# Kernel tuning notes

Measured on AMD Instinct MI355X. Metric: run time of the kernel, lower is better.

## Reference

```python
import jax, jax.numpy as jnp
import numpy as np

EMBED_DIM = 128
NUM_SYMBOLS = 200000
PAD = NUM_SYMBOLS
B = 1024          # query batch
FEW = 5           # support set size
NB = 200          # neighbors per entity (fixed by module docstring)
D_MODEL = 2 * EMBED_DIM       # 256
D_INNER = 2 * D_MODEL         # 512
HID = 2 * D_MODEL             # LSTMCell hidden = 2*input_dim = 512
STEPS = 4                     # process_steps
LN_EPS = 1e-5


def setup_inputs() -> dict:
    key = jax.random.key(0)
    ks = jax.random.split(key, 16)

    def conn(k, n):
        c = jax.random.randint(k, (n, NB, 2), 0, NUM_SYMBOLS, dtype=jnp.int64)
        # pad last 50 neighbor slots so the masked max-pool path is exercised
        return c.at[:, 150:, :].set(PAD)

    inp = {
        "query_left_connections": conn(ks[0], B),
        "query_right_connections": conn(ks[1], B),
        "support_left_connections": conn(ks[2], FEW),
        "support_right_connections": conn(ks[3], FEW),
        "query_left_degrees": jax.random.randint(ks[4], (B,), 1, NB, dtype=jnp.int32),
        "query_right_degrees": jax.random.randint(ks[5], (B,), 1, NB, dtype=jnp.int32),
        "support_left_degrees": jax.random.randint(ks[6], (FEW,), 1, NB, dtype=jnp.int32),
        "support_right_degrees": jax.random.randint(ks[7], (FEW,), 1, NB, dtype=jnp.int32),
    }

    # parameters (eval mode: dropout disabled)
    emb = jax.random.normal(ks[8], (NUM_SYMBOLS + 1, EMBED_DIM), jnp.float32) * 0.02
    inp["emb"] = emb.at[PAD].set(0.0)              # padding_idx row is zero
    inp["gcn_W"] = jax.random.normal(ks[9], (EMBED_DIM, 2 * EMBED_DIM), jnp.float32) * 0.05
    inp["gcn_wb"] = jnp.zeros((EMBED_DIM,), jnp.float32)   # gcn_w linear bias
    inp["gcn_b"] = jnp.zeros((EMBED_DIM,), jnp.float32)    # extra gcn_b param (init constant 0)
    inp["proj1_W"] = jax.random.normal(ks[10], (D_INNER, D_MODEL), jnp.float32) * 0.05
    inp["proj1_b"] = jnp.zeros((D_INNER,), jnp.float32)
    inp["proj2_W"] = jax.random.normal(ks[11], (D_MODEL, D_INNER), jnp.float32) * 0.05
    inp["proj2_b"] = jnp.zeros((D_MODEL,), jnp.float32)
    inp["ln_g"] = jnp.ones((D_MODEL,), jnp.float32)
    inp["ln_b"] = jnp.zeros((D_MODEL,), jnp.float32)
    inp["W_ih"] = jax.random.normal(ks[12], (4 * HID, D_MODEL), jnp.float32) * 0.04
    inp["W_hh"] = jax.random.normal(ks[13], (4 * HID, HID), jnp.float32) * 0.04
    inp["b_ih"] = jnp.zeros((4 * HID,), jnp.float32)
    inp["b_hh"] = jnp.zeros((4 * HID,), jnp.float32)
    return inp


def _neighbor_encoder(conn, emb, gcn_W, gcn_wb, gcn_b):
    # conn: (n, NB, 2) ints; gather embed + concat + linear + leaky_relu + masked max + tanh
    rel, ent = conn[:, :, 0], conn[:, :, 1]
    pad_mask = (rel == PAD) | (ent == PAD)                      # (n, NB)
    x = jnp.concatenate([emb[rel], emb[ent]], axis=-1)          # (n, NB, 2E)
    p = jnp.einsum('nke,de->nkd', x, gcn_W) + gcn_wb + gcn_b    # (n, NB, E)
    p = jax.nn.leaky_relu(p, negative_slope=0.1)
    p = jnp.where(pad_mask[:, :, None], -jnp.inf, p)
    return jnp.tanh(jnp.max(p, axis=1))                         # (n, E)


def _support_encoder(x, p1W, p1b, p2W, p2b, g, b):
    # FFN with residual + LayerNorm (GMatching SupportEncoder), dropout off in eval
    h = jax.nn.relu(x @ p1W.T + p1b)
    o = h @ p2W.T + p2b + x
    mu = jnp.mean(o, axis=-1, keepdims=True)
    var = jnp.var(o, axis=-1, keepdims=True)
    return (o - mu) / jnp.sqrt(var + LN_EPS) * g + b


def _query_encoder(support, query, W_ih, W_hh, b_ih, b_hh):
    # GMatching QueryEncoder: LSTMCell attention, `process_steps` iterations
    # support: (1, D_MODEL), query: (bq, D_MODEL)
    bq = query.shape[0]
    h_r = jnp.zeros((bq, HID), query.dtype)
    c = jnp.zeros((bq, HID), query.dtype)
    h = query
    for _ in range(STEPS):
        gates = query @ W_ih.T + b_ih + h_r @ W_hh.T + b_hh     # (bq, 4*HID)
        i, f, g, o = jnp.split(gates, 4, axis=-1)
        c = jax.nn.sigmoid(f) * c + jax.nn.sigmoid(i) * jnp.tanh(g)
        h_new = jax.nn.sigmoid(o) * jnp.tanh(c)                 # (bq, HID)
        h = query + h_new[:, :D_MODEL]
        attn = jax.nn.softmax(h @ support.T, axis=1)            # (bq, 1)
        r = attn @ support                                      # (bq, D_MODEL)
        h_r = jnp.concatenate([h, r], axis=1)
    return h


def reference(query_left_connections, query_right_connections,
              support_left_connections, support_right_connections,
              query_left_degrees, query_right_degrees,
              support_left_degrees, support_right_degrees,
              emb, gcn_W, gcn_wb, gcn_b,
              proj1_W, proj1_b, proj2_W, proj2_b, ln_g, ln_b,
              W_ih, W_hh, b_ih, b_hh):
    ql = _neighbor_encoder(query_left_connections, emb, gcn_W, gcn_wb, gcn_b)
    qr = _neighbor_encoder(query_right_connections, emb, gcn_W, gcn_wb, gcn_b)
    sl = _neighbor_encoder(support_left_connections, emb, gcn_W, gcn_wb, gcn_b)
    sr = _neighbor_encoder(support_right_connections, emb, gcn_W, gcn_wb, gcn_b)
    query_neighbor = jnp.concatenate([ql, qr], axis=-1)      # (B, D_MODEL)
    support_neighbor = jnp.concatenate([sl, sr], axis=-1)    # (FEW, D_MODEL)

    support_g = _support_encoder(support_neighbor[None], proj1_W, proj1_b, proj2_W, proj2_b, ln_g, ln_b)
    support_g = jnp.mean(support_g, axis=1)                  # (1, D_MODEL)
    query_g = _support_encoder(query_neighbor[:, None, :], proj1_W, proj1_b, proj2_W, proj2_b, ln_g, ln_b)
    query_g = query_g[:, 0, :]                               # (B, D_MODEL)

    query_f = _query_encoder(support_g, query_g, W_ih, W_hh, b_ih, b_hh)  # (B, D_MODEL)
    return (query_f @ support_g.T)[:, 0]                     # (B,)
```

## Files before the change

kernel.cpp:

```cpp
#include <hip/hip_runtime.h>
#include <math.h>

#define EMBED   128
#define DMODEL  256
#define DINNER  512
#define HIDN    512
#define NBK     200
#define BQ      1024
#define FEW     5
#define PAD_IDX 200000
#define LN_EPS  1e-5f
#define NTILES  7

typedef short          s16x4  __attribute__((ext_vector_type(4)));
typedef short          s16x8  __attribute__((ext_vector_type(8)));
typedef float          f32x4  __attribute__((ext_vector_type(4)));
typedef float          f32x16 __attribute__((ext_vector_type(16)));
typedef unsigned int   u32;
typedef unsigned short u16;

__device__ __forceinline__ float sigmoidf_(float x) { return 1.0f / (1.0f + expf(-x)); }

__device__ __forceinline__ u32 f2bf(float f) {
    u32 u = __builtin_bit_cast(u32, f);
    u += 0x7fffu + ((u >> 16) & 1u);
    return u >> 16;
}
__device__ __forceinline__ s16x8 pack8(float4 a, float4 b) {
    typedef u32 u32x4_ __attribute__((ext_vector_type(4)));
    u32x4_ q;
    q.x = f2bf(a.x) | (f2bf(a.y) << 16);
    q.y = f2bf(a.z) | (f2bf(a.w) << 16);
    q.z = f2bf(b.x) | (f2bf(b.y) << 16);
    q.w = f2bf(b.z) | (f2bf(b.w) << 16);
    return __builtin_bit_cast(s16x8, q);
}

__global__ __launch_bounds__(256) void convert_weights_kernel(
    const float* __restrict__ W_ih, const float* __restrict__ W_hh,
    const float* __restrict__ p1W,  const float* __restrict__ p2W,
    u16* __restrict__ wih_bf, u16* __restrict__ whh_bf,
    u16* __restrict__ p1_bf,  u16* __restrict__ p2_bf)
{
    int gid = blockIdx.x * 256 + threadIdx.x;
    const float* src; u16* dst; int local, stride, KS, liveRemap;
    if (gid < 32768)      { local = gid;          src = W_ih; dst = wih_bf; stride = 256; KS = 8;  liveRemap = 1; }
    else if (gid < 65536) { local = gid - 32768;  src = W_hh; dst = whh_bf; stride = 512; KS = 8;  liveRemap = 1; }
    else if (gid < 81920) { local = gid - 65536;  src = p1W;  dst = p1_bf;  stride = 256; KS = 8;  liveRemap = 0; }
    else                  { local = gid - 81920;  src = p2W;  dst = p2_bf;  stride = 512; KS = 16; liveRemap = 0; }
    int lane = local & 63;
    int ts   = local >> 6;
    int ks   = ts & (KS - 1);
    int tile = ts / KS;
    int n  = tile * 16 + (lane & 15);
    int kb = ks * 32 + (lane >> 4) * 8;
    int row = liveRemap ? ((n >> 8) * 512 + (n & 255)) : n;
    const float* sp = src + (size_t)row * stride + kb;
    float4 x0 = *(const float4*)sp;
    float4 x1 = *(const float4*)(sp + 4);
    *(s16x8*)(dst + (size_t)local * 8) = pack8(x0, x1);
}

__global__ __launch_bounds__(256) void neighbor_kernel(
    const int* __restrict__ qlc, const int* __restrict__ qrc,
    const int* __restrict__ slc, const int* __restrict__ src_,
    const float* __restrict__ emb, const float* __restrict__ W,
    const float* __restrict__ wb,  const float* __restrict__ bb,
    float* __restrict__ qn, float* __restrict__ sn)
{
    int b = blockIdx.x;
    const int* conn; float* out; int n; int side;
    if (b < BQ)                { conn = qlc;  n = b;            side = 0; out = qn; }
    else if (b < 2*BQ)         { conn = qrc;  n = b - BQ;       side = 1; out = qn; }
    else if (b < 2*BQ + FEW)   { conn = slc;  n = b - 2*BQ;     side = 0; out = sn; }
    else                       { conn = src_; n = b - 2*BQ-FEW; side = 1; out = sn; }

    int t = threadIdx.x;
    int w = t >> 6, l = t & 63;
    int d0 = w * 32;
    int m31 = l & 31, half = l >> 5;

    __shared__ __align__(16) u32 bs[64 * 66];

    s16x8 afrag[16];
    const float* wrow = W + (d0 + m31) * DMODEL + half * 8;
    #pragma unroll
    for (int ks = 0; ks < 16; ++ks) {
        float4 x0 = *(const float4*)(wrow + ks * 16);
        float4 x1 = *(const float4*)(wrow + ks * 16 + 4);
        afrag[ks] = pack8(x0, x1);
    }

    const int* crow = conn + n * NBK * 2;
    u32 vmask = 0;
    #pragma unroll
    for (int nt = 0; nt < NTILES; ++nt) {
        int krow = nt * 32 + m31;
        if (krow < NBK) {
            int rel = crow[2 * krow], ent = crow[2 * krow + 1];
            if (rel != PAD_IDX && ent != PAD_IDX) vmask |= (1u << nt);
        }
    }

    int gr = t >> 2;
    int gq = t & 3;
    int g_is_ent = (gr >= 32);
    int g_m = gr & 31;

    int srcrow[NTILES];
    #pragma unroll
    for (int nt = 0; nt < NTILES; ++nt) {
        int krow = nt * 32 + g_m;
        int rel = PAD_IDX, ent = PAD_IDX;
        if (krow < NBK) { rel = crow[2 * krow]; ent = crow[2 * krow + 1]; }
        int gvalid = (rel != PAD_IDX) && (ent != PAD_IDX);
        srcrow[nt] = gvalid ? (g_is_ent ? ent : rel) : PAD_IDX;
    }

    int tl[NTILES]; int ntl = 0;
    #pragma unroll
    for (int nt = 0; nt < NTILES; ++nt)
        if (__any((int)((vmask >> nt) & 1u))) tl[ntl++] = nt;

    float vm[16];
    #pragma unroll
    for (int r = 0; r < 16; ++r) vm[r] = -INFINITY;

    u32* dst = bs + gr * 66 + gq * 16;
    const u32* rrel = bs + m31 * 66 + half * 4;
    const u32* rent = bs + (32 + m31) * 66 + half * 4;

    float4 f[8];
    if (ntl > 0) {
        const float4* gp = (const float4*)(emb + (size_t)srcrow[tl[0]] * EMBED + gq * 32);
        #pragma unroll
        for (int i = 0; i < 8; ++i) f[i] = gp[i];
    }

    for (int i = 0; i < ntl; ++i) {
        int nt = tl[i];
        __syncthreads();
        #pragma unroll
        for (int j = 0; j < 8; ++j) {
            dst[2 * j]     = f2bf(f[j].x) | (f2bf(f[j].y) << 16);
            dst[2 * j + 1] = f2bf(f[j].z) | (f2bf(f[j].w) << 16);
        }
        __syncthreads();

        float4 f2[8];
        if (i + 1 < ntl) {
            const float4* gp = (const float4*)(emb + (size_t)srcrow[tl[i + 1]] * EMBED + gq * 32);
            #pragma unroll
            for (int j = 0; j < 8; ++j) f2[j] = gp[j];
        }

        f32x16 acc0 = {0.f,0.f,0.f,0.f,0.f,0.f,0.f,0.f,0.f,0.f,0.f,0.f,0.f,0.f,0.f,0.f};
        f32x16 acc1 = acc0;
        #pragma unroll
        for (int ks = 0; ks < 8; ++ks) {
            s16x4 lo = *(const s16x4*)(rrel + ks * 8);
            s16x4 hi = *(const s16x4*)(rrel + ks * 8 + 2);
            s16x8 bf = __builtin_shufflevector(lo, hi, 0, 1, 2, 3, 4, 5, 6, 7);
            acc0 = __builtin_amdgcn_mfma_f32_32x32x16_bf16(afrag[ks], bf, acc0, 0, 0, 0);
        }
        #pragma unroll
        for (int ks = 0; ks < 8; ++ks) {
            s16x4 lo = *(const s16x4*)(rent + ks * 8);
            s16x4 hi = *(const s16x4*)(rent + ks * 8 + 2);
            s16x8 bf = __builtin_shufflevector(lo, hi, 0, 1, 2, 3, 4, 5, 6, 7);
            acc1 = __builtin_amdgcn_mfma_f32_32x32x16_bf16(afrag[8 + ks], bf, acc1, 0, 0, 0);
        }
        int cvalid = (vmask >> nt) & 1;
        #pragma unroll
        for (int r = 0; r < 16; ++r) {
            float v = cvalid ? (acc0[r] + acc1[r]) : -INFINITY;
            vm[r] = fmaxf(vm[r], v);
        }
        #pragma unroll
        for (int j = 0; j < 8; ++j) f[j] = f2[j];
    }

    #pragma unroll
    for (int off = 1; off < 32; off <<= 1) {
        #pragma unroll
        for (int r = 0; r < 16; ++r)
            vm[r] = fmaxf(vm[r], __shfl_xor(vm[r], off, 64));
    }

    if (m31 == 0) {
        #pragma unroll
        for (int r = 0; r < 16; ++r) {
            int d = d0 + (r & 3) + 8 * (r >> 2) + 4 * half;
            float p = vm[r] + wb[d] + bb[d];
            p = (p >= 0.f) ? p : 0.1f * p;
            out[n * DMODEL + side * EMBED + d] = tanhf(p);
        }
    }
}

__global__ __launch_bounds__(256) void support_enc_kernel(
    const float* __restrict__ qn, const float* __restrict__ sn,
    const u16* __restrict__ p1_bf, const float* __restrict__ p1b,
    const u16* __restrict__ p2_bf, const float* __restrict__ p2b,
    const float* __restrict__ lng, const float* __restrict__ lnb,
    float* __restrict__ query_g, float* __restrict__ sup_ln)
{
    __shared__ __align__(16) float xs[16][260];
    __shared__ __align__(16) float hsd[16][516];
    __shared__ __align__(16) float os[16][260];
    int t = threadIdx.x;
    int w = t >> 6, l = t & 63;
    int r0 = blockIdx.x * 16;

    for (int r = 0; r < 16; ++r) {
        int row = r0 + r;
        float v = 0.f;
        if (row < BQ + FEW)
            v = (row < BQ) ? qn[row * DMODEL + t] : sn[(row - BQ) * DMODEL + t];
        xs[r][t] = v;
    }
    __syncthreads();

    int am = l & 15, ak = (l >> 4) * 8;

    s16x8 a1[8];
    #pragma unroll
    for (int ks = 0; ks < 8; ++ks) {
        float4 x0 = *(const float4*)&xs[am][ks * 32 + ak];
        float4 x1 = *(const float4*)&xs[am][ks * 32 + ak + 4];
        a1[ks] = pack8(x0, x1);
    }

    #pragma unroll
    for (int j = 0; j < 8; ++j) {
        int nt = w * 8 + j;
        f32x4 acc = {0.f, 0.f, 0.f, 0.f};
        const u16* bp = p1_bf + (size_t)nt * 4096 + l * 8;
        #pragma unroll
        for (int ks = 0; ks < 8; ++ks) {
            s16x8 bf = *(const s16x8*)(bp + ks * 512);
            acc = __builtin_amdgcn_mfma_f32_16x16x32_bf16(a1[ks], bf, acc, 0, 0, 0);
        }
        int nn = nt * 16 + (l & 15);
        float bj = p1b[nn];
        #pragma unroll
        for (int reg = 0; reg < 4; ++reg) {
            int m = (l >> 4) * 4 + reg;
            hsd[m][nn] = fmaxf(acc[reg] + bj, 0.f);
        }
    }
    __syncthreads();

    s16x8 a2[16];
    #pragma unroll
    for (int ks = 0; ks < 16; ++ks) {
        float4 x0 = *(const float4*)&hsd[am][ks * 32 + ak];
        float4 x1 = *(const float4*)&hsd[am][ks * 32 + ak + 4];
        a2[ks] = pack8(x0, x1);
    }

    #pragma unroll
    for (int j = 0; j < 4; ++j) {
        int nt = w * 4 + j;
        f32x4 acc = {0.f, 0.f, 0.f, 0.f};
        const u16* bp = p2_bf + (size_t)nt * 8192 + l * 8;
        #pragma unroll
        for (int ks = 0; ks < 16; ++ks) {
            s16x8 bf = *(const s16x8*)(bp + ks * 512);
            acc = __builtin_amdgcn_mfma_f32_16x16x32_bf16(a2[ks], bf, acc, 0, 0, 0);
        }
        int nn = nt * 16 + (l & 15);
        float bj = p2b[nn];
        #pragma unroll
        for (int reg = 0; reg < 4; ++reg) {
            int m = (l >> 4) * 4 + reg;
            os[m][nn] = acc[reg] + bj + xs[m][nn];
        }
    }
    __syncthreads();

    for (int j = 0; j < 4; ++j) {
        int m = w * 4 + j;
        float sum = 0.f, sq = 0.f;
        #pragma unroll
        for (int i = 0; i < 4; ++i) {
            float v = os[m][l + 64 * i];
            sum += v; sq += v * v;
        }
        for (int off = 32; off; off >>= 1) {
            sum += __shfl_xor(sum, off, 64);
            sq  += __shfl_xor(sq,  off, 64);
        }
        float mu  = sum * (1.f / DMODEL);
        float var = sq * (1.f / DMODEL) - mu * mu;
        float inv = rsqrtf(var + LN_EPS);
        int row = r0 + m;
        if (row < BQ + FEW) {
            float* outp = (row < BQ) ? (query_g + row * DMODEL) : (sup_ln + (row - BQ) * DMODEL);
            #pragma unroll
            for (int i = 0; i < 4; ++i) {
                int dd = l + 64 * i;
                outp[dd] = (os[m][dd] - mu) * inv * lng[dd] + lnb[dd];
            }
        }
    }
}

__global__ __launch_bounds__(256) void sWp_kernel(
    const float* __restrict__ sup_ln, const float* __restrict__ W_hh,
    float* __restrict__ sWp)
{
    int w = threadIdx.x >> 6, l = threadIdx.x & 63;
    int wave_id = blockIdx.x * 4 + w;
    float se[4];
    #pragma unroll
    for (int j = 0; j < 4; ++j) {
        float a = 0.f;
        for (int i = 0; i < FEW; ++i) a += sup_ln[i * DMODEL + l + 64 * j];
        se[j] = a * (1.f / FEW);
    }
    for (int i = 0; i < 4; ++i) {
        int p = wave_id * 4 + i;
        int pp = p >> 8, q = p & 255;
        const float* wr = W_hh + (size_t)(pp * 512 + q) * HIDN + 256;
        float part = 0.f;
        #pragma unroll
        for (int j = 0; j < 4; ++j) part += se[j] * wr[l + 64 * j];
        for (int off = 32; off; off >>= 1) part += __shfl_xor(part, off, 64);
        if (l == 0) sWp[p] = part;
    }
}

__global__ __launch_bounds__(256) void lstm_mfma_kernel(
    const float* __restrict__ query_g, const float* __restrict__ sup_ln,
    const float* __restrict__ sWp, const u16* __restrict__ wih_bf,
    const u16* __restrict__ whh_bf, const float* __restrict__ b_ih,
    const float* __restrict__ b_hh, float* __restrict__ out)
{
    __shared__ __align__(16) float qs[16][260];
    __shared__ __align__(16) float hs[16][260];
    __shared__ float sv[DMODEL];
    int t = threadIdx.x;
    int w = t >> 6, l = t & 63;
    int n0 = blockIdx.x * 16;

    {
        float a = 0.f;
        for (int i = 0; i < FEW; ++i) a += sup_ln[i * DMODEL + t];
        sv[t] = a * (1.f / FEW);
    }
    for (int r = 0; r < 16; ++r) qs[r][t] = query_g[(size_t)(n0 + r) * DMODEL + t];
    __syncthreads();

    int am = l & 15, ak = (l >> 4) * 8;

    s16x8 af[8];
    #pragma unroll
    for (int ks = 0; ks < 8; ++ks) {
        float4 x0 = *(const float4*)&qs[am][ks * 32 + ak];
        float4 x1 = *(const float4*)&qs[am][ks * 32 + ak + 4];
        af[ks] = pack8(x0, x1);
    }

    f32x4 base[4][4];
    #pragma unroll
    for (int pp = 0; pp < 4; ++pp) {
        #pragma unroll
        for (int qt = 0; qt < 4; ++qt) {
            int tp = pp * 16 + w * 4 + qt;
            f32x4 acc = {0.f, 0.f, 0.f, 0.f};
            const u16* bp = wih_bf + (size_t)tp * 4096 + l * 8;
            #pragma unroll
            for (int ks = 0; ks < 8; ++ks) {
                s16x8 bf = *(const s16x8*)(bp + ks * 512);
                acc = __builtin_amdgcn_mfma_f32_16x16x32_bf16(af[ks], bf, acc, 0, 0, 0);
            }
            base[pp][qt] = acc;
        }
    }
    #pragma unroll
    for (int pp = 0; pp < 4; ++pp) {
        #pragma unroll
        for (int qt = 0; qt < 4; ++qt) {
            int q = w * 64 + qt * 16 + (l & 15);
            float bsv = b_ih[pp * 512 + q] + b_hh[pp * 512 + q];
            base[pp][qt].x += bsv; base[pp][qt].y += bsv;
            base[pp][qt].z += bsv; base[pp][qt].w += bsv;
        }
    }

    float c[4][4];
    #pragma unroll
    for (int qt = 0; qt < 4; ++qt) {
        int q = w * 64 + qt * 16 + (l & 15);
        #pragma unroll
        for (int reg = 0; reg < 4; ++reg) {
            int m = (l >> 4) * 4 + reg;
            float gi = base[0][qt][reg];
            float gg = base[2][qt][reg];
            float go = base[3][qt][reg];
            float cc = sigmoidf_(gi) * tanhf(gg);
            c[qt][reg] = cc;
            hs[m][q] = qs[m][q] + sigmoidf_(go) * tanhf(cc);
        }
    }
    #pragma unroll
    for (int pp = 0; pp < 4; ++pp) {
        #pragma unroll
        for (int qt = 0; qt < 4; ++qt) {
            int q = w * 64 + qt * 16 + (l & 15);
            float sw = sWp[pp * 256 + q];
            base[pp][qt].x += sw; base[pp][qt].y += sw;
            base[pp][qt].z += sw; base[pp][qt].w += sw;
        }
    }
    __syncthreads();

    for (int st = 1; st < 4; ++st) {
        #pragma unroll
        for (int ks = 0; ks < 8; ++ks) {
            float4 x0 = *(const float4*)&hs[am][ks * 32 + ak];
            float4 x1 = *(const float4*)&hs[am][ks * 32 + ak + 4];
            af[ks] = pack8(x0, x1);
        }
        __syncthreads();

        f32x4 gacc[4][4];
        #pragma unroll
        for (int pp = 0; pp < 4; ++pp) {
            #pragma unroll
            for (int qt = 0; qt < 4; ++qt) {
                int tp = pp * 16 + w * 4 + qt;
                f32x4 acc = base[pp][qt];
                const u16* bp = whh_bf + (size_t)tp * 4096 + l * 8;
                #pragma unroll
                for (int ks = 0; ks < 8; ++ks) {
                    s16x8 bf = *(const s16x8*)(bp + ks * 512);
                    acc = __builtin_amdgcn_mfma_f32_16x16x32_bf16(af[ks], bf, acc, 0, 0, 0);
                }
                gacc[pp][qt] = acc;
            }
        }
        #pragma unroll
        for (int qt = 0; qt < 4; ++qt) {
            int q = w * 64 + qt * 16 + (l & 15);
            #pragma unroll
            for (int reg = 0; reg < 4; ++reg) {
                int m = (l >> 4) * 4 + reg;
                float gi = gacc[0][qt][reg];
                float gf = gacc[1][qt][reg];
                float gg = gacc[2][qt][reg];
                float go = gacc[3][qt][reg];
                float cc = sigmoidf_(gf) * c[qt][reg] + sigmoidf_(gi) * tanhf(gg);
                c[qt][reg] = cc;
                hs[m][q] = qs[m][q] + sigmoidf_(go) * tanhf(cc);
            }
        }
        __syncthreads();
    }

    for (int j = 0; j < 4; ++j) {
        int m = w * 4 + j;
        float part = 0.f;
        #pragma unroll
        for (int i = 0; i < 4; ++i) {
            int e = l + 64 * i;
            part += hs[m][e] * sv[e];
        }
        for (int off = 32; off; off >>= 1) part += __shfl_xor(part, off, 64);
        if (l == 0) out[n0 + m] = part;
    }
}

extern "C" void kernel_launch(void* const* d_in, const int* in_sizes, int n_in,
                              void* d_out, int out_size, void* d_ws, size_t ws_size,
                              hipStream_t stream)
{
    const int*   qlc  = (const int*)d_in[0];
    const int*   qrc  = (const int*)d_in[1];
    const int*   slc  = (const int*)d_in[2];
    const int*   src_ = (const int*)d_in[3];
    const float* emb   = (const float*)d_in[8];
    const float* gcnW  = (const float*)d_in[9];
    const float* gcnwb = (const float*)d_in[10];
    const float* gcnb  = (const float*)d_in[11];
    const float* p1W   = (const float*)d_in[12];
    const float* p1b   = (const float*)d_in[13];
    const float* p2W   = (const float*)d_in[14];
    const float* p2b   = (const float*)d_in[15];
    const float* lng   = (const float*)d_in[16];
    const float* lnb   = (const float*)d_in[17];
    const float* W_ih  = (const float*)d_in[18];
    const float* W_hh  = (const float*)d_in[19];
    const float* b_ih  = (const float*)d_in[20];
    const float* b_hh  = (const float*)d_in[21];
    float* out = (float*)d_out;

    char* ws = (char*)d_ws;
    float* qn      = (float*)(ws + 0);
    float* sn      = (float*)(ws + 1048576);
    float* query_g = (float*)(ws + 1053696);
    float* sup_ln  = (float*)(ws + 2102272);
    float* sWp     = (float*)(ws + 2107392);
    u16*   wih_bf  = (u16*)(ws + 2111488);
    u16*   whh_bf  = (u16*)(ws + 2635776);
    u16*   p1_bf   = (u16*)(ws + 3160064);
    u16*   p2_bf   = (u16*)(ws + 3422208);
    (void)ws_size; (void)in_sizes; (void)n_in; (void)out_size;

    convert_weights_kernel<<<384, 256, 0, stream>>>(
        W_ih, W_hh, p1W, p2W, wih_bf, whh_bf, p1_bf, p2_bf);
    neighbor_kernel<<<2 * BQ + 2 * FEW, 256, 0, stream>>>(
        qlc, qrc, slc, src_, emb, gcnW, gcnwb, gcnb, qn, sn);
    support_enc_kernel<<<(BQ + FEW + 15) / 16, 256, 0, stream>>>(
        qn, sn, p1_bf, p1b, p2_bf, p2b, lng, lnb, query_g, sup_ln);
    sWp_kernel<<<64, 256, 0, stream>>>(sup_ln, W_hh, sWp);
    lstm_mfma_kernel<<<BQ / 16, 256, 0, stream>>>(
        query_g, sup_ln, sWp, wih_bf, whh_bf, b_ih, b_hh, out);
}
```

Baseline: 410.8 us.

## Gather bf16 embeddings directly into MFMA fragments and widen encoder/LSTM blocks

```diff
diff --git a/kernel.cpp b/kernel.cpp
--- a/kernel.cpp
+++ b/kernel.cpp
@@ -12,7 +12,10 @@
 #define LN_EPS  1e-5f
 #define NTILES  7
 
-typedef short          s16x4  __attribute__((ext_vector_type(4)));
+#define EMB_ELEMS 25600128
+#define EMB_THREADS (EMB_ELEMS / 8)
+#define EMB_BLOCKS ((EMB_THREADS + 255) / 256)
+
 typedef short          s16x8  __attribute__((ext_vector_type(8)));
 typedef float          f32x4  __attribute__((ext_vector_type(4)));
 typedef float          f32x16 __attribute__((ext_vector_type(16)));
@@ -36,13 +39,26 @@
     return __builtin_bit_cast(s16x8, q);
 }
 
-__global__ __launch_bounds__(256) void convert_weights_kernel(
+__global__ __launch_bounds__(256) void convert_all_kernel(
     const float* __restrict__ W_ih, const float* __restrict__ W_hh,
     const float* __restrict__ p1W,  const float* __restrict__ p2W,
+    const float* __restrict__ emb,
     u16* __restrict__ wih_bf, u16* __restrict__ whh_bf,
-    u16* __restrict__ p1_bf,  u16* __restrict__ p2_bf)
+    u16* __restrict__ p1_bf,  u16* __restrict__ p2_bf,
+    u16* __restrict__ emb_bf)
 {
-    int gid = blockIdx.x * 256 + threadIdx.x;
+    int bid = blockIdx.x;
+    if (bid >= 384) {
+        size_t gid = (size_t)(bid - 384) * 256 + threadIdx.x;
+        if (gid < EMB_THREADS) {
+            size_t base = gid * 8;
+            float4 x0 = *(const float4*)(emb + base);
+            float4 x1 = *(const float4*)(emb + base + 4);
+            *(s16x8*)(emb_bf + base) = pack8(x0, x1);
+        }
+        return;
+    }
+    int gid = bid * 256 + threadIdx.x;
     const float* src; u16* dst; int local, stride, KS, liveRemap;
     if (gid < 32768)      { local = gid;          src = W_ih; dst = wih_bf; stride = 256; KS = 8;  liveRemap = 1; }
     else if (gid < 65536) { local = gid - 32768;  src = W_hh; dst = whh_bf; stride = 512; KS = 8;  liveRemap = 1; }
@@ -61,10 +77,12 @@
     *(s16x8*)(dst + (size_t)local * 8) = pack8(x0, x1);
 }
 
+template<bool BF>
 __global__ __launch_bounds__(256) void neighbor_kernel(
     const int* __restrict__ qlc, const int* __restrict__ qrc,
     const int* __restrict__ slc, const int* __restrict__ src_,
-    const float* __restrict__ emb, const float* __restrict__ W,
+    const float* __restrict__ emb, const u16* __restrict__ emb_bf,
+    const float* __restrict__ W,
     const float* __restrict__ wb,  const float* __restrict__ bb,
     float* __restrict__ qn, float* __restrict__ sn)
 {
@@ -80,8 +98,6 @@
     int d0 = w * 32;
     int m31 = l & 31, half = l >> 5;
 
-    __shared__ __align__(16) u32 bs[64 * 66];
-
     s16x8 afrag[16];
     const float* wrow = W + (d0 + m31) * DMODEL + half * 8;
     #pragma unroll
@@ -91,93 +107,57 @@
         afrag[ks] = pack8(x0, x1);
     }
 
-    const int* crow = conn + n * NBK * 2;
+    const int2* crow = (const int2*)(conn + n * NBK * 2);
+    int srel[NTILES], sent[NTILES];
     u32 vmask = 0;
     #pragma unroll
     for (int nt = 0; nt < NTILES; ++nt) {
         int krow = nt * 32 + m31;
-        if (krow < NBK) {
-            int rel = crow[2 * krow], ent = crow[2 * krow + 1];
-            if (rel != PAD_IDX && ent != PAD_IDX) vmask |= (1u << nt);
-        }
-    }
-
-    int gr = t >> 2;
-    int gq = t & 3;
-    int g_is_ent = (gr >= 32);
-    int g_m = gr & 31;
-
-    int srcrow[NTILES];
-    #pragma unroll
+        int rel = PAD_IDX, ent = PAD_IDX;
+        if (krow < NBK) { int2 re = crow[krow]; rel = re.x; ent = re.y; }
+        int v = (rel != PAD_IDX) && (ent != PAD_IDX);
+        if (v) vmask |= (1u << nt);
+        srel[nt] = v ? rel : PAD_IDX;
+        sent[nt] = v ? ent : PAD_IDX;
+    }
+
+    float vm[16];
+    #pragma unroll
+    for (int r = 0; r < 16; ++r) vm[r] = -INFINITY;
+
     for (int nt = 0; nt < NTILES; ++nt) {
-        int krow = nt * 32 + g_m;
-        int rel = PAD_IDX, ent = PAD_IDX;
-        if (krow < NBK) { rel = crow[2 * krow]; ent = crow[2 * krow + 1]; }
-        int gvalid = (rel != PAD_IDX) && (ent != PAD_IDX);
-        srcrow[nt] = gvalid ? (g_is_ent ? ent : rel) : PAD_IDX;
-    }
-
-    int tl[NTILES]; int ntl = 0;
-    #pragma unroll
-    for (int nt = 0; nt < NTILES; ++nt)
-        if (__any((int)((vmask >> nt) & 1u))) tl[ntl++] = nt;
-
-    float vm[16];
-    #pragma unroll
-    for (int r = 0; r < 16; ++r) vm[r] = -INFINITY;
-
-    u32* dst = bs + gr * 66 + gq * 16;
-    const u32* rrel = bs + m31 * 66 + half * 4;
-    const u32* rent = bs + (32 + m31) * 66 + half * 4;
-
-    float4 f[8];
-    if (ntl > 0) {
-        const float4* gp = (const float4*)(emb + (size_t)srcrow[tl[0]] * EMBED + gq * 32);
-        #pragma unroll
-        for (int i = 0; i < 8; ++i) f[i] = gp[i];
-    }
-
-    for (int i = 0; i < ntl; ++i) {
-        int nt = tl[i];
-        __syncthreads();
-        #pragma unroll
-        for (int j = 0; j < 8; ++j) {
-            dst[2 * j]     = f2bf(f[j].x) | (f2bf(f[j].y) << 16);
-            dst[2 * j + 1] = f2bf(f[j].z) | (f2bf(f[j].w) << 16);
-        }
-        __syncthreads();
-
-        float4 f2[8];
-        if (i + 1 < ntl) {
-            const float4* gp = (const float4*)(emb + (size_t)srcrow[tl[i + 1]] * EMBED + gq * 32);
-            #pragma unroll
-            for (int j = 0; j < 8; ++j) f2[j] = gp[j];
-        }
-
-        f32x16 acc0 = {0.f,0.f,0.f,0.f,0.f,0.f,0.f,0.f,0.f,0.f,0.f,0.f,0.f,0.f,0.f,0.f};
-        f32x16 acc1 = acc0;
-        #pragma unroll
-        for (int ks = 0; ks < 8; ++ks) {
-            s16x4 lo = *(const s16x4*)(rrel + ks * 8);
-            s16x4 hi = *(const s16x4*)(rrel + ks * 8 + 2);
-            s16x8 bf = __builtin_shufflevector(lo, hi, 0, 1, 2, 3, 4, 5, 6, 7);
-            acc0 = __builtin_amdgcn_mfma_f32_32x32x16_bf16(afrag[ks], bf, acc0, 0, 0, 0);
-        }
-        #pragma unroll
-        for (int ks = 0; ks < 8; ++ks) {
-            s16x4 lo = *(const s16x4*)(rent + ks * 8);
-            s16x4 hi = *(const s16x4*)(rent + ks * 8 + 2);
-            s16x8 bf = __builtin_shufflevector(lo, hi, 0, 1, 2, 3, 4, 5, 6, 7);
-            acc1 = __builtin_amdgcn_mfma_f32_32x32x16_bf16(afrag[8 + ks], bf, acc1, 0, 0, 0);
-        }
-        int cvalid = (vmask >> nt) & 1;
+        if (!__any((int)((vmask >> nt) & 1u))) continue;
+
+        s16x8 bfr[16];
+        if (BF) {
+            const u16* pr = emb_bf + (size_t)srel[nt] * EMBED + half * 8;
+            const u16* pe = emb_bf + (size_t)sent[nt] * EMBED + half * 8;
+            #pragma unroll
+            for (int ks = 0; ks < 8; ++ks) bfr[ks]     = *(const s16x8*)(pr + ks * 16);
+            #pragma unroll
+            for (int ks = 0; ks < 8; ++ks) bfr[8 + ks] = *(const s16x8*)(pe + ks * 16);
+        } else {
+            const float* pr = emb + (size_t)srel[nt] * EMBED + half * 8;
+            const float* pe = emb + (size_t)sent[nt] * EMBED + half * 8;
+            #pragma unroll
+            for (int ks = 0; ks < 8; ++ks)
+                bfr[ks] = pack8(*(const float4*)(pr + ks * 16), *(const float4*)(pr + ks * 16 + 4));
+            #pragma unroll
+            for (int ks = 0; ks < 8; ++ks)
+                bfr[8 + ks] = pack8(*(const float4*)(pe + ks * 16), *(const float4*)(pe + ks * 16 + 4));
+        }
+
+        f32x16 acc = {0.f,0.f,0.f,0.f,0.f,0.f,0.f,0.f,0.f,0.f,0.f,0.f,0.f,0.f,0.f,0.f};
+        #pragma unroll
+        for (int j = 0; j < 16; ++j)
+            acc = __builtin_amdgcn_mfma_f32_32x32x16_bf16(afrag[j], bfr[j], acc, 0, 0, 0);
+
+        int cv = (vmask >> nt) & 1;
         #pragma unroll
         for (int r = 0; r < 16; ++r) {
-            float v = cvalid ? (acc0[r] + acc1[r]) : -INFINITY;
+            float v = cv ? acc[r] : -INFINITY;
             vm[r] = fmaxf(vm[r], v);
         }
-        #pragma unroll
-        for (int j = 0; j < 8; ++j) f[j] = f2[j];
     }
 
     #pragma unroll
@@ -198,7 +178,7 @@
     }
 }
 
-__global__ __launch_bounds__(256) void support_enc_kernel(
+__global__ __launch_bounds__(512) void support_enc_kernel(
     const float* __restrict__ qn, const float* __restrict__ sn,
     const u16* __restrict__ p1_bf, const float* __restrict__ p1b,
     const u16* __restrict__ p2_bf, const float* __restrict__ p2b,
@@ -212,12 +192,15 @@
     int w = t >> 6, l = t & 63;
     int r0 = blockIdx.x * 16;
 
-    for (int r = 0; r < 16; ++r) {
+    #pragma unroll
+    for (int j = 0; j < 8; ++j) {
+        int idx = j * 512 + t;
+        int r = idx >> 8, cc = idx & 255;
         int row = r0 + r;
         float v = 0.f;
         if (row < BQ + FEW)
-            v = (row < BQ) ? qn[row * DMODEL + t] : sn[(row - BQ) * DMODEL + t];
-        xs[r][t] = v;
+            v = (row < BQ) ? qn[(size_t)row * DMODEL + cc] : sn[(size_t)(row - BQ) * DMODEL + cc];
+        xs[r][cc] = v;
     }
     __syncthreads();
 
@@ -232,8 +215,8 @@
     }
 
     #pragma unroll
-    for (int j = 0; j < 8; ++j) {
-        int nt = w * 8 + j;
+    for (int j = 0; j < 4; ++j) {
+        int nt = w * 4 + j;
         f32x4 acc = {0.f, 0.f, 0.f, 0.f};
         const u16* bp = p1_bf + (size_t)nt * 4096 + l * 8;
         #pragma unroll
@@ -260,8 +243,8 @@
     }
 
     #pragma unroll
-    for (int j = 0; j < 4; ++j) {
-        int nt = w * 4 + j;
+    for (int j = 0; j < 2; ++j) {
+        int nt = w * 2 + j;
         f32x4 acc = {0.f, 0.f, 0.f, 0.f};
         const u16* bp = p2_bf + (size_t)nt * 8192 + l * 8;
         #pragma unroll
@@ -279,8 +262,8 @@
     }
     __syncthreads();
 
-    for (int j = 0; j < 4; ++j) {
-        int m = w * 4 + j;
+    for (int j = 0; j < 2; ++j) {
+        int m = w * 2 + j;
         float sum = 0.f, sq = 0.f;
         #pragma unroll
         for (int i = 0; i < 4; ++i) {
@@ -296,7 +279,7 @@
         float inv = rsqrtf(var + LN_EPS);
         int row = r0 + m;
         if (row < BQ + FEW) {
-            float* outp = (row < BQ) ? (query_g + row * DMODEL) : (sup_ln + (row - BQ) * DMODEL);
+            float* outp = (row < BQ) ? (query_g + (size_t)row * DMODEL) : (sup_ln + (size_t)(row - BQ) * DMODEL);
             #pragma unroll
             for (int i = 0; i < 4; ++i) {
                 int dd = l + 64 * i;
@@ -331,7 +314,7 @@
     }
 }
 
-__global__ __launch_bounds__(256) void lstm_mfma_kernel(
+__global__ __launch_bounds__(512) void lstm_mfma_kernel(
     const float* __restrict__ query_g, const float* __restrict__ sup_ln,
     const float* __restrict__ sWp, const u16* __restrict__ wih_bf,
     const u16* __restrict__ whh_bf, const float* __restrict__ b_ih,
@@ -344,12 +327,17 @@
     int w = t >> 6, l = t & 63;
     int n0 = blockIdx.x * 16;
 
-    {
+    if (t < DMODEL) {
         float a = 0.f;
         for (int i = 0; i < FEW; ++i) a += sup_ln[i * DMODEL + t];
         sv[t] = a * (1.f / FEW);
     }
-    for (int r = 0; r < 16; ++r) qs[r][t] = query_g[(size_t)(n0 + r) * DMODEL + t];
+    #pragma unroll
+    for (int j = 0; j < 8; ++j) {
+        int idx = j * 512 + t;
+        int r = idx >> 8, cc = idx & 255;
+        qs[r][cc] = query_g[(size_t)(n0 + r) * DMODEL + cc];
+    }
     __syncthreads();
 
     int am = l & 15, ak = (l >> 4) * 8;
@@ -362,12 +350,12 @@
         af[ks] = pack8(x0, x1);
     }
 
-    f32x4 base[4][4];
+    f32x4 base[4][2];
     #pragma unroll
     for (int pp = 0; pp < 4; ++pp) {
         #pragma unroll
-        for (int qt = 0; qt < 4; ++qt) {
-            int tp = pp * 16 + w * 4 + qt;
+        for (int qt = 0; qt < 2; ++qt) {
+            int tp = pp * 16 + 2 * w + qt;
             f32x4 acc = {0.f, 0.f, 0.f, 0.f};
             const u16* bp = wih_bf + (size_t)tp * 4096 + l * 8;
             #pragma unroll
@@ -381,18 +369,18 @@
     #pragma unroll
     for (int pp = 0; pp < 4; ++pp) {
         #pragma unroll
-        for (int qt = 0; qt < 4; ++qt) {
-            int q = w * 64 + qt * 16 + (l & 15);
+        for (int qt = 0; qt < 2; ++qt) {
+            int q = w * 32 + qt * 16 + (l & 15);
             float bsv = b_ih[pp * 512 + q] + b_hh[pp * 512 + q];
             base[pp][qt].x += bsv; base[pp][qt].y += bsv;
             base[pp][qt].z += bsv; base[pp][qt].w += bsv;
         }
     }
 
-    float c[4][4];
-    #pragma unroll
-    for (int qt = 0; qt < 4; ++qt) {
-        int q = w * 64 + qt * 16 + (l & 15);
+    float c[2][4];
+    #pragma unroll
+    for (int qt = 0; qt < 2; ++qt) {
+        int q = w * 32 + qt * 16 + (l & 15);
         #pragma unroll
         for (int reg = 0; reg < 4; ++reg) {
             int m = (l >> 4) * 4 + reg;
@@ -407,8 +395,8 @@
     #pragma unroll
     for (int pp = 0; pp < 4; ++pp) {
         #pragma unroll
-        for (int qt = 0; qt < 4; ++qt) {
-            int q = w * 64 + qt * 16 + (l & 15);
+        for (int qt = 0; qt < 2; ++qt) {
+            int q = w * 32 + qt * 16 + (l & 15);
             float sw = sWp[pp * 256 + q];
             base[pp][qt].x += sw; base[pp][qt].y += sw;
             base[pp][qt].z += sw; base[pp][qt].w += sw;
@@ -425,12 +413,12 @@
         }
         __syncthreads();
 
-        f32x4 gacc[4][4];
+        f32x4 gacc[4][2];
         #pragma unroll
         for (int pp = 0; pp < 4; ++pp) {
             #pragma unroll
-            for (int qt = 0; qt < 4; ++qt) {
-                int tp = pp * 16 + w * 4 + qt;
+            for (int qt = 0; qt < 2; ++qt) {
+                int tp = pp * 16 + 2 * w + qt;
                 f32x4 acc = base[pp][qt];
                 const u16* bp = whh_bf + (size_t)tp * 4096 + l * 8;
                 #pragma unroll
@@ -442,8 +430,8 @@
             }
         }
         #pragma unroll
-        for (int qt = 0; qt < 4; ++qt) {
-            int q = w * 64 + qt * 16 + (l & 15);
+        for (int qt = 0; qt < 2; ++qt) {
+            int q = w * 32 + qt * 16 + (l & 15);
             #pragma unroll
             for (int reg = 0; reg < 4; ++reg) {
                 int m = (l >> 4) * 4 + reg;
@@ -459,8 +447,8 @@
         __syncthreads();
     }
 
-    for (int j = 0; j < 4; ++j) {
-        int m = w * 4 + j;
+    for (int j = 0; j < 2; ++j) {
+        int m = w * 2 + j;
         float part = 0.f;
         #pragma unroll
         for (int i = 0; i < 4; ++i) {
@@ -506,15 +494,23 @@
     u16*   whh_bf  = (u16*)(ws + 2635776);
     u16*   p1_bf   = (u16*)(ws + 3160064);
     u16*   p2_bf   = (u16*)(ws + 3422208);
-    (void)ws_size; (void)in_sizes; (void)n_in; (void)out_size;
-
-    convert_weights_kernel<<<384, 256, 0, stream>>>(
-        W_ih, W_hh, p1W, p2W, wih_bf, whh_bf, p1_bf, p2_bf);
-    neighbor_kernel<<<2 * BQ + 2 * FEW, 256, 0, stream>>>(
-        qlc, qrc, slc, src_, emb, gcnW, gcnwb, gcnb, qn, sn);
-    support_enc_kernel<<<(BQ + FEW + 15) / 16, 256, 0, stream>>>(
+    u16*   emb_bf  = (u16*)(ws + 3684352);
+    (void)in_sizes; (void)n_in; (void)out_size;
+
+    bool have_emb = ws_size >= (size_t)3684352 + (size_t)EMB_ELEMS * 2;
+    int grid_conv = 384 + (have_emb ? EMB_BLOCKS : 0);
+
+    convert_all_kernel<<<grid_conv, 256, 0, stream>>>(
+        W_ih, W_hh, p1W, p2W, emb, wih_bf, whh_bf, p1_bf, p2_bf, emb_bf);
+    if (have_emb)
+        neighbor_kernel<true><<<2 * BQ + 2 * FEW, 256, 0, stream>>>(
+            qlc, qrc, slc, src_, emb, emb_bf, gcnW, gcnwb, gcnb, qn, sn);
+    else
+        neighbor_kernel<false><<<2 * BQ + 2 * FEW, 256, 0, stream>>>(
+            qlc, qrc, slc, src_, emb, emb_bf, gcnW, gcnwb, gcnb, qn, sn);
+    support_enc_kernel<<<(BQ + FEW + 15) / 16, 512, 0, stream>>>(
         qn, sn, p1_bf, p1b, p2_bf, p2b, lng, lnb, query_g, sup_ln);
     sWp_kernel<<<64, 256, 0, stream>>>(sup_ln, W_hh, sWp);
-    lstm_mfma_kernel<<<BQ / 16, 256, 0, stream>>>(
+    lstm_mfma_kernel<<<BQ / 16, 512, 0, stream>>>(
         query_g, sup_ln, sWp, wih_bf, whh_bf, b_ih, b_hh, out);
 }
```

After: 404.4 us. No clear change (-1.5%).
